# Kernel tuning notes

Measured on AMD Instinct MI355X. Metric: run time of the kernel, lower is better.

Reference implementation:

```python
import jax, jax.numpy as jnp
import numpy as np

B, C, D = 16, 64, 256          # batch, channels, spatial dim (square input)
K, S, P = 2, 2, 0              # kernel_size, stride, padding
HO = (D + 2 * P - K) // S + 1  # 128


def _build_gather_idx():
    """Precompute the flat pixel indices gathered for each output position.

    Mirrors DeformMaxPool2d.__init__ + the per-(i,j) work in forward():
      1. calculate_index_pool -> top-left corner of each pooling window
      2. new_perm (ImageScrambler on the output grid) scrambles the index map
      3. get_index_pool expands each corner into the KxK window coordinates
      4. retrieve_original_pixels maps each coordinate through perm (pixel-level
         ImageScrambler permutation)
    Result: int array [HO, HO, K*K] of flattened indices into H*W.
    """
    rng = np.random.RandomState(0)
    # 1) window corner indices (calculate_index_pool)
    base = np.arange(-P + K // 2 - 1, D - P + K // 2 - 1, S)  # [HO]
    ci, cj = np.meshgrid(base, base, indexing="ij")           # [HO,HO] each
    centers = np.stack([ci, cj], axis=-1)                     # [HO,HO,2]
    # 2) scramble output-grid positions (new_perm)
    out_perm = rng.permutation(HO * HO)
    centers = centers.reshape(HO * HO, 2)[out_perm].reshape(HO, HO, 2)
    # 3) expand to KxK window coords (get_index_pool ordering: i-major, j-minor)
    offs = np.array([[i, j] for i in range(K) for j in range(K)])  # [K*K,2]
    coords = centers[:, :, None, :] + offs[None, None, :, :]       # [HO,HO,K*K,2]
    flat = coords[..., 0] * D + coords[..., 1]                     # [HO,HO,K*K]
    # 4) map through pixel-level permutation (perm / retrieve_original_pixels)
    pix_perm = rng.permutation(D * D)
    return pix_perm[flat].astype(np.int64)


def setup_inputs() -> dict:
    key = jax.random.key(0)
    x = jax.random.normal(key, (B, C, D, D), dtype=jnp.float32)
    gather_idx = jnp.asarray(_build_gather_idx())  # [HO,HO,K*K] int64
    return {"x": x, "gather_idx": gather_idx}


def reference(x, gather_idx):
    # Fused gather + max: equivalent to the nested (i,j) loops of
    # DeformMaxPool2d.forward, fully vectorized.
    b, c, h, w = x.shape
    x_flat = x.reshape(b, c, h * w)               # [B,C,H*W]
    gathered = x_flat[:, :, gather_idx]           # [B,C,HO,HO,K*K]
    return jnp.max(gathered, axis=-1)             # [B,C,HO,HO]
```

## Files before the change

kernel.cpp:

```cpp
#include <hip/hip_runtime.h>


#define D_DIM     256
#define HO        128
#define PLANE_IN  (D_DIM * D_DIM)
#define PLANE_OUT (HO * HO)
#define NPLANES   (16 * 64)
#define TPB       1024

typedef float    f32x4 __attribute__((ext_vector_type(4)));
typedef unsigned short u16x4 __attribute__((ext_vector_type(4)));

__device__ __forceinline__ unsigned int enc_f32(float f) {
    unsigned int b = __float_as_uint(f);
    return (b & 0x80000000u) ? ~b : (b | 0x80000000u);
}
__device__ __forceinline__ float dec_f32(unsigned int u) {
    unsigned int b = (u & 0x80000000u) ? (u & 0x7FFFFFFFu) : ~u;
    return __uint_as_float(b);
}

__global__ void init_inv_kernel(unsigned int* __restrict__ inv32) {
    int t = blockIdx.x * blockDim.x + threadIdx.x;
    if (t < PLANE_IN / 2) inv32[t] = 0xFFFFFFFFu;
}

__global__ void build_inv_kernel(const int* __restrict__ gidx,
                                 unsigned short* __restrict__ inv) {
    int t = blockIdx.x * blockDim.x + threadIdx.x;
    if (t >= PLANE_OUT) return;
    int4 g = reinterpret_cast<const int4*>(gidx)[t];
    unsigned short o = (unsigned short)t;
    inv[g.x] = o; inv[g.y] = o; inv[g.z] = o; inv[g.w] = o;
}

__launch_bounds__(TPB)
__global__ void pool_scatter_kernel(const float* __restrict__ x,
                                    const unsigned short* __restrict__ inv,
                                    float* __restrict__ out) {
    __shared__ unsigned int so[PLANE_OUT];
    const int tid = threadIdx.x;
    const int bc  = blockIdx.x;

    #pragma unroll
    for (int i = tid; i < PLANE_OUT; i += TPB) so[i] = 0u;
    __syncthreads();

    const f32x4* x4  = reinterpret_cast<const f32x4*>(x + (size_t)bc * PLANE_IN);
    const u16x4* iv4 = reinterpret_cast<const u16x4*>(inv);

    #pragma unroll 4
    for (int i = tid; i < PLANE_IN / 4; i += TPB) {
        f32x4 xv = __builtin_nontemporal_load(&x4[i]);
        u16x4 ov = iv4[i];
        if (ov.x != 0xFFFFu) atomicMax(&so[ov.x], enc_f32(xv.x));
        if (ov.y != 0xFFFFu) atomicMax(&so[ov.y], enc_f32(xv.y));
        if (ov.z != 0xFFFFu) atomicMax(&so[ov.z], enc_f32(xv.z));
        if (ov.w != 0xFFFFu) atomicMax(&so[ov.w], enc_f32(xv.w));
    }
    __syncthreads();

    f32x4* out4 = reinterpret_cast<f32x4*>(out + (size_t)bc * PLANE_OUT);
    #pragma unroll
    for (int i = tid; i < PLANE_OUT / 4; i += TPB) {
        unsigned int u0 = so[4 * i + 0], u1 = so[4 * i + 1];
        unsigned int u2 = so[4 * i + 2], u3 = so[4 * i + 3];
        f32x4 r = { dec_f32(u0), dec_f32(u1), dec_f32(u2), dec_f32(u3) };
        __builtin_nontemporal_store(r, &out4[i]);
    }
}

__global__ void pool_gather_kernel(const float* __restrict__ x,
                                   const int* __restrict__ gidx,
                                   float* __restrict__ out) {
    long long t = (long long)blockIdx.x * blockDim.x + threadIdx.x;
    if (t >= (long long)NPLANES * PLANE_OUT) return;
    int pos = (int)(t & (PLANE_OUT - 1));
    int bc  = (int)(t >> 14);
    int4 g = reinterpret_cast<const int4*>(gidx)[pos];
    const float* xp = x + (size_t)bc * PLANE_IN;
    float m = fmaxf(fmaxf(xp[g.x], xp[g.y]), fmaxf(xp[g.z], xp[g.w]));
    out[t] = m;
}

extern "C" void kernel_launch(void* const* d_in, const int* in_sizes, int n_in,
                              void* d_out, int out_size, void* d_ws, size_t ws_size,
                              hipStream_t stream) {
    const float* x    = (const float*)d_in[0];
    const int*   gidx = (const int*)d_in[1];
    float*       out  = (float*)d_out;

    if (ws_size >= (size_t)PLANE_IN * sizeof(unsigned short)) {
        unsigned short* inv = (unsigned short*)d_ws;
        init_inv_kernel<<<(PLANE_IN / 2 + 255) / 256, 256, 0, stream>>>((unsigned int*)d_ws);
        build_inv_kernel<<<PLANE_OUT / 256, 256, 0, stream>>>(gidx, inv);
        pool_scatter_kernel<<<NPLANES, TPB, 0, stream>>>(x, inv, out);
    } else {
        long long total = (long long)NPLANES * PLANE_OUT;
        pool_gather_kernel<<<(int)((total + 255) / 256), 256, 0, stream>>>(x, gidx, out);
    }
}
```

Measured before the change: 356.6 us.

## Replace LDS atomicMax scatter with phased slot-indexed scatter and max reduce

The inverse map now stores, for each input pixel, a unique slot (output index times four plus window position) instead of just the output index. The main kernel loads 64 values per thread into registers. It then runs four phases; in each one it writes the values for a quarter of the outputs into a 16K-float LDS buffer with plain stores, then reduces each group of four slots with fmaxf. This removes the LDS atomics and the float/uint encoding, and drops the sentinel init kernel, relying on every input pixel mapping to exactly one slot.

```diff
diff --git a/kernel.cpp b/kernel.cpp
--- a/kernel.cpp
+++ b/kernel.cpp
@@ -7,66 +7,64 @@
 #define PLANE_OUT (HO * HO)
 #define NPLANES   (16 * 64)
 #define TPB       1024
+#define PHASE_N   16384
 
-typedef float    f32x4 __attribute__((ext_vector_type(4)));
+typedef float          f32x4 __attribute__((ext_vector_type(4)));
 typedef unsigned short u16x4 __attribute__((ext_vector_type(4)));
-
-__device__ __forceinline__ unsigned int enc_f32(float f) {
-    unsigned int b = __float_as_uint(f);
-    return (b & 0x80000000u) ? ~b : (b | 0x80000000u);
-}
-__device__ __forceinline__ float dec_f32(unsigned int u) {
-    unsigned int b = (u & 0x80000000u) ? (u & 0x7FFFFFFFu) : ~u;
-    return __uint_as_float(b);
-}
-
-__global__ void init_inv_kernel(unsigned int* __restrict__ inv32) {
-    int t = blockIdx.x * blockDim.x + threadIdx.x;
-    if (t < PLANE_IN / 2) inv32[t] = 0xFFFFFFFFu;
-}
 
 __global__ void build_inv_kernel(const int* __restrict__ gidx,
                                  unsigned short* __restrict__ inv) {
     int t = blockIdx.x * blockDim.x + threadIdx.x;
     if (t >= PLANE_OUT) return;
     int4 g = reinterpret_cast<const int4*>(gidx)[t];
-    unsigned short o = (unsigned short)t;
-    inv[g.x] = o; inv[g.y] = o; inv[g.z] = o; inv[g.w] = o;
+    unsigned int e = 4u * (unsigned int)t;
+    inv[g.x] = (unsigned short)(e + 0);
+    inv[g.y] = (unsigned short)(e + 1);
+    inv[g.z] = (unsigned short)(e + 2);
+    inv[g.w] = (unsigned short)(e + 3);
 }
 
-__launch_bounds__(TPB)
-__global__ void pool_scatter_kernel(const float* __restrict__ x,
-                                    const unsigned short* __restrict__ inv,
-                                    float* __restrict__ out) {
-    __shared__ unsigned int so[PLANE_OUT];
+__launch_bounds__(TPB, 4)
+__global__ void pool_phase_kernel(const float* __restrict__ x,
+                                  const unsigned short* __restrict__ inv,
+                                  float* __restrict__ out) {
+    __shared__ float so[PHASE_N];
     const int tid = threadIdx.x;
     const int bc  = blockIdx.x;
-
-    #pragma unroll
-    for (int i = tid; i < PLANE_OUT; i += TPB) so[i] = 0u;
-    __syncthreads();
 
     const f32x4* x4  = reinterpret_cast<const f32x4*>(x + (size_t)bc * PLANE_IN);
     const u16x4* iv4 = reinterpret_cast<const u16x4*>(inv);
 
-    #pragma unroll 4
-    for (int i = tid; i < PLANE_IN / 4; i += TPB) {
-        f32x4 xv = __builtin_nontemporal_load(&x4[i]);
-        u16x4 ov = iv4[i];
-        if (ov.x != 0xFFFFu) atomicMax(&so[ov.x], enc_f32(xv.x));
-        if (ov.y != 0xFFFFu) atomicMax(&so[ov.y], enc_f32(xv.y));
-        if (ov.z != 0xFFFFu) atomicMax(&so[ov.z], enc_f32(xv.z));
-        if (ov.w != 0xFFFFu) atomicMax(&so[ov.w], enc_f32(xv.w));
+    f32x4 v[16];
+    u16x4 e[16];
+    #pragma unroll
+    for (int k = 0; k < 16; ++k) {
+        v[k] = __builtin_nontemporal_load(&x4[tid + k * TPB]);
+        e[k] = iv4[tid + k * TPB];
     }
-    __syncthreads();
 
-    f32x4* out4 = reinterpret_cast<f32x4*>(out + (size_t)bc * PLANE_OUT);
+    float* outp = out + (size_t)bc * PLANE_OUT;
+
     #pragma unroll
-    for (int i = tid; i < PLANE_OUT / 4; i += TPB) {
-        unsigned int u0 = so[4 * i + 0], u1 = so[4 * i + 1];
-        unsigned int u2 = so[4 * i + 2], u3 = so[4 * i + 3];
-        f32x4 r = { dec_f32(u0), dec_f32(u1), dec_f32(u2), dec_f32(u3) };
-        __builtin_nontemporal_store(r, &out4[i]);
+    for (int q = 0; q < 4; ++q) {
+        #pragma unroll
+        for (int k = 0; k < 16; ++k) {
+            #pragma unroll
+            for (int c = 0; c < 4; ++c) {
+                unsigned int ee = e[k][c];
+                if ((ee >> 14) == (unsigned int)q)
+                    so[ee & (PHASE_N - 1)] = v[k][c];
+            }
+        }
+        __syncthreads();
+        #pragma unroll
+        for (int m = 0; m < 4; ++m) {
+            int j = tid + m * TPB;
+            f32x4 w = *reinterpret_cast<const f32x4*>(&so[4 * j]);
+            float r = fmaxf(fmaxf(w.x, w.y), fmaxf(w.z, w.w));
+            __builtin_nontemporal_store(r, &outp[q * 4096 + j]);
+        }
+        __syncthreads();
     }
 }
 
@@ -92,9 +90,8 @@
 
     if (ws_size >= (size_t)PLANE_IN * sizeof(unsigned short)) {
         unsigned short* inv = (unsigned short*)d_ws;
-        init_inv_kernel<<<(PLANE_IN / 2 + 255) / 256, 256, 0, stream>>>((unsigned int*)d_ws);
         build_inv_kernel<<<PLANE_OUT / 256, 256, 0, stream>>>(gidx, inv);
-        pool_scatter_kernel<<<NPLANES, TPB, 0, stream>>>(x, inv, out);
+        pool_phase_kernel<<<NPLANES, TPB, 0, stream>>>(x, inv, out);
     } else {
         long long total = (long long)NPLANES * PLANE_OUT;
         pool_gather_kernel<<<(int)((total + 255) / 256), 256, 0, stream>>>(x, gidx, out);
```

Result: slower. 500.2 us (+40.3%).
